# Kernel tuning notes

Hardware: AMD Instinct MI355X
Metric: run time of the kernel (lower is better)

The kernel has to match this reference:

```python
import jax, jax.numpy as jnp
import numpy as np


def setup_inputs() -> dict:
    key = jax.random.key(0)
    k1, k2, k3 = jax.random.split(key, 3)
    N, C = 8192, 32000
    prob = jax.random.uniform(k1, (N, C), dtype=jnp.float32)
    target = jax.random.randint(k2, (N,), 0, C, dtype=jnp.int64)
    reward = jax.random.uniform(k3, (N,), dtype=jnp.float32)
    return {"prob": prob, "target": target, "reward": reward}


def reference(prob, target, reward):
    # Equivalent to: one_hot scatter -> masked_select -> * reward -> -sum
    # Fused: gather prob[i, target[i]] directly.
    picked = jnp.take_along_axis(prob, target[:, None], axis=1)[:, 0]  # (N,)
    return -jnp.sum(picked * reward)
```

## Files before the change

### kernel.cpp

```cpp
#include <hip/hip_runtime.h>
#include <hip/hip_bf16.h>


__global__ void ganloss_partial(const float* __restrict__ prob,
                                const int* __restrict__ target,
                                const float* __restrict__ reward,
                                float* __restrict__ ws,
                                int N, int C) {
    int i = blockIdx.x * blockDim.x + threadIdx.x;
    float v = 0.0f;
    if (i < N) {
        int t = target[i];
        v = prob[(size_t)i * (size_t)C + (size_t)t] * reward[i];
    }
    #pragma unroll
    for (int off = 32; off > 0; off >>= 1)
        v += __shfl_down(v, off, 64);

    __shared__ float smem[4];
    int lane = threadIdx.x & 63;
    int w    = threadIdx.x >> 6;
    if (lane == 0) smem[w] = v;
    __syncthreads();
    if (threadIdx.x == 0) {
        float s = smem[0] + smem[1] + smem[2] + smem[3];
        ws[blockIdx.x] = s;
    }
}

__global__ void ganloss_finalize(const float* __restrict__ ws,
                                 float* __restrict__ out,
                                 int nblocks) {
    float v = (threadIdx.x < nblocks) ? ws[threadIdx.x] : 0.0f;
    #pragma unroll
    for (int off = 32; off > 0; off >>= 1)
        v += __shfl_down(v, off, 64);
    if (threadIdx.x == 0) out[0] = -v;
}

extern "C" void kernel_launch(void* const* d_in, const int* in_sizes, int n_in,
                              void* d_out, int out_size, void* d_ws, size_t ws_size,
                              hipStream_t stream) {
    const float* prob   = (const float*)d_in[0];
    const int*   target = (const int*)d_in[1];
    const float* reward = (const float*)d_in[2];
    float* out = (float*)d_out;
    float* ws  = (float*)d_ws;

    const int N = in_sizes[1];
    const int C = in_sizes[0] / N;

    const int block = 256;
    const int nblocks = (N + block - 1) / block;

    ganloss_partial<<<nblocks, block, 0, stream>>>(prob, target, reward, ws, N, C);
    ganloss_finalize<<<1, 64, 0, stream>>>(ws, out, nblocks);
}
```

Baseline: 11.50 us.

## Fuse partial and final reduction into one single-block kernel with batched gathers

Replaces the two-kernel reduction (32 blocks of partials plus a finalize launch) with a single 1024-thread block that loops over all rows. Each thread issues 8 independent target/reward loads and then 8 gathered prob loads, so several memory requests are in flight at once. The single block writes the negated sum directly, which removes one kernel launch and the workspace round trip. The trade-off is that all 8192 scattered gathers now run on one compute unit instead of spreading across 32 blocks.

```diff
diff --git a/kernel.cpp b/kernel.cpp
--- a/kernel.cpp
+++ b/kernel.cpp
@@ -2,40 +2,56 @@
 #include <hip/hip_bf16.h>
 
 
-__global__ void ganloss_partial(const float* __restrict__ prob,
-                                const int* __restrict__ target,
-                                const float* __restrict__ reward,
-                                float* __restrict__ ws,
-                                int N, int C) {
-    int i = blockIdx.x * blockDim.x + threadIdx.x;
-    float v = 0.0f;
-    if (i < N) {
-        int t = target[i];
-        v = prob[(size_t)i * (size_t)C + (size_t)t] * reward[i];
+#define BLK 1024
+#define RPT 8
+
+__global__ __launch_bounds__(BLK) void ganloss_fused(
+    const float* __restrict__ prob,
+    const int* __restrict__ target,
+    const float* __restrict__ reward,
+    float* __restrict__ out,
+    int N, int C) {
+    const int tid = threadIdx.x;
+
+    float acc = 0.0f;
+    for (int base = 0; base < N; base += BLK * RPT) {
+        int   idx[RPT];
+        float rw[RPT];
+        float p[RPT];
+        #pragma unroll
+        for (int k = 0; k < RPT; ++k) {
+            int i = base + k * BLK + tid;
+            bool ok = (i < N);
+            idx[k] = ok ? target[i] : 0;
+            rw[k]  = ok ? reward[i] : 0.0f;
+        }
+        #pragma unroll
+        for (int k = 0; k < RPT; ++k) {
+            int i = base + k * BLK + tid;
+            p[k] = (i < N) ? prob[(size_t)i * (size_t)C + (size_t)idx[k]] : 0.0f;
+        }
+        #pragma unroll
+        for (int k = 0; k < RPT; ++k)
+            acc += p[k] * rw[k];
     }
+
     #pragma unroll
     for (int off = 32; off > 0; off >>= 1)
-        v += __shfl_down(v, off, 64);
+        acc += __shfl_down(acc, off, 64);
 
-    __shared__ float smem[4];
-    int lane = threadIdx.x & 63;
-    int w    = threadIdx.x >> 6;
-    if (lane == 0) smem[w] = v;
+    __shared__ float smem[BLK / 64];
+    const int lane = tid & 63;
+    const int w    = tid >> 6;
+    if (lane == 0) smem[w] = acc;
     __syncthreads();
-    if (threadIdx.x == 0) {
-        float s = smem[0] + smem[1] + smem[2] + smem[3];
-        ws[blockIdx.x] = s;
+
+    if (w == 0) {
+        float v = (lane < BLK / 64) ? smem[lane] : 0.0f;
+        #pragma unroll
+        for (int off = 8; off > 0; off >>= 1)
+            v += __shfl_down(v, off, 64);
+        if (lane == 0) out[0] = -v;
     }
-}
-
-__global__ void ganloss_finalize(const float* __restrict__ ws,
-                                 float* __restrict__ out,
-                                 int nblocks) {
-    float v = (threadIdx.x < nblocks) ? ws[threadIdx.x] : 0.0f;
-    #pragma unroll
-    for (int off = 32; off > 0; off >>= 1)
-        v += __shfl_down(v, off, 64);
-    if (threadIdx.x == 0) out[0] = -v;
 }
 
 extern "C" void kernel_launch(void* const* d_in, const int* in_sizes, int n_in,
@@ -45,14 +61,9 @@
     const int*   target = (const int*)d_in[1];
     const float* reward = (const float*)d_in[2];
     float* out = (float*)d_out;
-    float* ws  = (float*)d_ws;
 
     const int N = in_sizes[1];
     const int C = in_sizes[0] / N;
 
-    const int block = 256;
-    const int nblocks = (N + block - 1) / block;
-
-    ganloss_partial<<<nblocks, block, 0, stream>>>(prob, target, reward, ws, N, C);
-    ganloss_finalize<<<1, 64, 0, stream>>>(ws, out, nblocks);
+    ganloss_fused<<<1, BLK, 0, stream>>>(prob, target, reward, out, N, C);
 }
```

Measured after the change: 11.49 us. No clear change (-0.0%).
